# Kernel optimization log

Measured on AMD Instinct MI355X. Metric: run time of the kernel, lower is better.

The kernel has to match this reference:

```python
import jax, jax.numpy as jnp
import numpy as np

N = 8192          # tokens
CD = 512          # coarse_dim
FD = 512          # fine_dim
CB = 4096         # coarse codebook size
FB = 8192         # fine codebook size
COST = 0.25       # commitment cost
LRELU = 0.1
EPS = 1e-5


def _vq(x, emb):
    # squared-distance cdist: [n, K]
    d = jnp.sum(x * x, axis=1, keepdims=True) + jnp.sum(emb * emb, axis=1) - 2.0 * (x @ emb.T)
    idx = jnp.argmin(d, axis=1)          # temperature=1.0 (updates=0); scaling doesn't change argmin
    q = emb[idx]                          # gather == one-hot @ emb, without materializing one-hot
    e_loss = jnp.mean((jax.lax.stop_gradient(q) - x) ** 2)
    q_loss = jnp.mean((q - jax.lax.stop_gradient(x)) ** 2)
    loss = q_loss + COST * e_loss
    q_st = x + jax.lax.stop_gradient(q - x)   # straight-through
    return q_st, loss


def _mlp(x, w, b, g, be):
    # Linear (torch: x @ W.T + b) -> LayerNorm -> LeakyReLU(0.1)
    h = x @ w.T + b
    m = jnp.mean(h, axis=-1, keepdims=True)
    v = jnp.var(h, axis=-1, keepdims=True)
    h = (h - m) / jnp.sqrt(v + EPS) * g + be
    return jnp.where(h > 0, h, LRELU * h)


def setup_inputs() -> dict:
    key = jax.random.key(0)
    ks = jax.random.split(key, 6)
    xav_c = float(np.sqrt(6.0 / (CB + CD)))
    xav_f = float(np.sqrt(6.0 / (FB + FD)))
    lin_s = float(np.sqrt(1.0 / CD))
    return {
        'z': jax.random.normal(ks[0], (N, CD + FD), dtype=jnp.float32),
        'coarse_emb': jax.random.uniform(ks[1], (CB, CD), jnp.float32, -xav_c, xav_c),
        'fine_emb': jax.random.uniform(ks[2], (FB, FD), jnp.float32, -xav_f, xav_f),
        'w_c2f': jax.random.uniform(ks[3], (FD, CD), jnp.float32, -lin_s, lin_s),
        'b_c2f': jnp.zeros((FD,), jnp.float32),
        'g_c2f': jnp.ones((FD,), jnp.float32),
        'be_c2f': jnp.zeros((FD,), jnp.float32),
        'w_f2c': jax.random.uniform(ks[4], (CD, FD), jnp.float32, -lin_s, lin_s),
        'b_f2c': jnp.zeros((CD,), jnp.float32),
        'g_f2c': jnp.ones((CD,), jnp.float32),
        'be_f2c': jnp.zeros((CD,), jnp.float32),
        'gate_c_raw': jnp.float32(0.5),
        'gate_f_raw': jnp.float32(0.5),
    }


def reference(z, coarse_emb, fine_emb, w_c2f, b_c2f, g_c2f, be_c2f,
              w_f2c, b_f2c, g_f2c, be_f2c, gate_c_raw, gate_f_raw):
    split = z.shape[1] // 2
    z_coarse, z_fine = z[:, :split], z[:, split:]

    z_coarse_q, coarse_loss = _vq(z_coarse, coarse_emb)
    coarse_influence = _mlp(jax.lax.stop_gradient(z_coarse_q), w_c2f, b_c2f, g_c2f, be_c2f)
    gate_c = jax.nn.sigmoid(gate_c_raw)

    residual = z_fine - gate_c * coarse_influence
    z_fine_q, fine_loss = _vq(residual, fine_emb)

    fine_feedback = _mlp(jax.lax.stop_gradient(z_fine_q), w_f2c, b_f2c, g_f2c, be_f2c)
    gate_f = jax.nn.sigmoid(gate_f_raw)

    z_coarse_corrected = z_coarse_q + 0.1 * gate_f * fine_feedback
    z_fine_reconstructed = z_fine_q + gate_c * coarse_influence
    z_hierarchical = jnp.concatenate([z_coarse_corrected, z_fine_reconstructed], axis=1)
    vq_loss = coarse_loss + fine_loss
    return z_hierarchical, vq_loss
```

## Files before the change

kernel.cpp:

```cpp
#include <hip/hip_runtime.h>
#include <hip/hip_bf16.h>
#include <cstdint>
#include <cstddef>

#define KD 512

#define OFF_CN   0u
#define OFF_FN   16384u
#define OFF_ZN   49152u
#define OFF_RN   81920u
#define OFF_LOSS 114688u
#define OFF_AMC  114944u
#define OFF_AMF  180480u
#define OFF_CEH  246016u
#define OFF_CEL  4440320u
#define OFF_FEH  8634624u
#define OFF_FEL  17023232u
#define OFF_ZCH  25411840u
#define OFF_ZCL  33800448u
#define OFF_RH   42189056u
#define OFF_RL   50577664u
#define OFF_W1H  58966272u
#define OFF_W1L  59490560u
#define OFF_W2H  60014848u
#define OFF_W2L  60539136u
#define OFF_H    61063424u
#define OFF_INFL 77840640u


typedef __attribute__((ext_vector_type(8))) short bf16x8;
typedef __attribute__((ext_vector_type(4))) float f32x4;
typedef unsigned long long u64;

__device__ __forceinline__ bf16x8 as_bf16x8(int4 v) {
  union { int4 i; bf16x8 b; } u; u.i = v; return u.b;
}

__device__ __forceinline__ void gl_lds16(const void* g, void* l) {
  __builtin_amdgcn_global_load_lds(
      (const __attribute__((address_space(1))) void*)g,
      (__attribute__((address_space(3))) void*)l, 16, 0, 0);
}

__device__ __forceinline__ float block_sum(float v, float* sred) {
#pragma unroll
  for (int off = 32; off > 0; off >>= 1) v += __shfl_down(v, off, 64);
  if ((threadIdx.x & 63) == 0) sred[threadIdx.x >> 6] = v;
  __syncthreads();
  float r = sred[0] + sred[1] + sred[2] + sred[3];
  __syncthreads();
  return r;
}

__device__ __forceinline__ float sigmoidf_(float x) { return 1.0f / (1.0f + expf(-x)); }

__device__ __forceinline__ void split_bf16(float v, __hip_bfloat16* hi, __hip_bfloat16* lo) {
  __hip_bfloat16 h = __float2bfloat16(v);
  *hi = h;
  *lo = __float2bfloat16(v - __bfloat162float(h));
}

__device__ __forceinline__ unsigned enc_sortable(float f) {
  unsigned u = __float_as_uint(f);
  return (u & 0x80000000u) ? ~u : (u | 0x80000000u);
}
__device__ __forceinline__ float dec_sortable(unsigned ub) {
  unsigned o = (ub & 0x80000000u) ? (ub & 0x7fffffffu) : ~ub;
  return __uint_as_float(o);
}
__device__ __forceinline__ u64 umin64(u64 a, u64 b) { return a < b ? a : b; }
__device__ __forceinline__ u64 umax64(u64 a, u64 b) { return a > b ? a : b; }

__device__ __forceinline__ void merge3(u64& a1, u64& a2, u64& a3, u64 b1, u64 b2, u64 b3) {
  u64 p = umax64(a1, b1);
  u64 q = umin64(a2, b2);
  u64 r = umax64(a2, b2);
  u64 s = umin64(a3, b3);
  u64 m1 = umin64(a1, b1);
  u64 m2 = umin64(p, q);
  u64 m3 = umin64(umin64(umax64(p, q), r), s);
  a1 = m1; a2 = m2; a3 = m3;
}

__global__ __launch_bounds__(256) void prep(
    const float* __restrict__ ce, const float* __restrict__ fe, const float* __restrict__ z,
    const float* __restrict__ w1, const float* __restrict__ w2,
    float* __restrict__ cn, float* __restrict__ fn, float* __restrict__ zn,
    __hip_bfloat16* __restrict__ ceH, __hip_bfloat16* __restrict__ ceL,
    __hip_bfloat16* __restrict__ feH, __hip_bfloat16* __restrict__ feL,
    __hip_bfloat16* __restrict__ zcH,
    __hip_bfloat16* __restrict__ w1H, __hip_bfloat16* __restrict__ w1L,
    __hip_bfloat16* __restrict__ w2H, __hip_bfloat16* __restrict__ w2L,
    float* __restrict__ lossp) {
  __shared__ float sred[4];
  const int b = blockIdx.x, t = threadIdx.x;
  const float* src;
  float* nd = nullptr;
  __hip_bfloat16 *dh = nullptr, *dl = nullptr;
  int fragMode = 0, hiOnly = 0;
  size_t row;
  if (b < 4096) {
    row = b; src = ce + row * KD; nd = cn + row; dh = ceH; dl = ceL; fragMode = 1;
  } else if (b < 12288) {
    row = b - 4096; src = fe + row * KD; nd = fn + row; dh = feH; dl = feL; fragMode = 1;
  } else if (b < 20480) {
    row = b - 12288; src = z + row * 1024; nd = zn + row; dh = zcH; hiOnly = 1;
  } else if (b < 20992) {
    row = b - 20480; src = w1 + row * KD; dh = w1H; dl = w1L;
  } else {
    row = b - 20992; src = w2 + row * KD; dh = w2H; dl = w2L;
  }
  float acc = 0.0f;
  if (fragMode) {
    float v0 = src[t], v1 = src[t + 256];
    acc = v0 * v0 + v1 * v1;
  } else {
#pragma unroll
    for (int j = 0; j < 2; ++j) {
      int c = t + j * 256;
      float v = src[c];
      acc += v * v;
      __hip_bfloat16 h, l;
      split_bf16(v, &h, &l);
      dh[row * KD + c] = h;
      if (!hiOnly) dl[row * KD + c] = l;
    }
  }
  if (nd) {
    float s = block_sum(acc, sred);
    if (t == 0) nd[0] = s;
  } else {
    __syncthreads();
    __syncthreads();
  }
  if (fragMode && t < 64) {
    union { int4 i; __hip_bfloat16 s[8]; } ph, pl;
#pragma unroll
    for (int j = 0; j < 8; ++j) {
      float v = src[8 * t + j];
      split_bf16(v, &ph.s[j], &pl.s[j]);
    }
    const int chunkIdx = (int)(((row >> 4) * 16 + (t >> 2)) * 64 +
                               ((size_t)((t & 3) << 4) | (row & 15)));
    ((int4*)dh)[chunkIdx] = ph.i;
    ((int4*)dl)[chunkIdx] = pl.i;
  }
  if (b == 20480 && t == 0) lossp[0] = 0.0f;
}

__global__ __launch_bounds__(256, 2) void vq10(
    const int4* __restrict__ AfH,
    const __hip_bfloat16* __restrict__ Bh,
    const float* __restrict__ cn,
    u64* __restrict__ bkeys) {
  __shared__ __align__(16) int4 sA[3][1024];
  __shared__ __align__(16) __hip_bfloat16 sB[3][128 * 32];
  const int t = threadIdx.x;
  const int w = t >> 6, l = t & 63;

  const int bx = blockIdx.x;
  const int by = blockIdx.y;
  const int rowTile = by << 8;
  const int colTile = bx << 7;
  const int NB = gridDim.y;

  const int rl = l >> 2;
  const int sbp = (l & 3) ^ ((l >> 3) & 3);
  const size_t gOff0 = (size_t)(colTile + (w << 5) + rl) * KD + (sbp << 3);
  const size_t gOff1 = gOff0 + (size_t)16 * KD;
  const int lOffB0 = (w << 5) << 5;
  const int lOffB1 = lOffB0 + (16 << 5);

  const int rtg = rowTile >> 4;
  const int aS0 = ((rtg + 4 * w + 0) << 10) + l;
  const int aS1 = ((rtg + 4 * w + 1) << 10) + l;
  const int aS2 = ((rtg + 4 * w + 2) << 10) + l;
  const int aS3 = ((rtg + 4 * w + 3) << 10) + l;

  const int fr = l & 15;
  const int q = l >> 4;

  f32x4 acc[4][8];
#pragma unroll
  for (int i = 0; i < 4; ++i)
#pragma unroll
    for (int j = 0; j < 8; ++j) acc[i][j] = (f32x4){0.f, 0.f, 0.f, 0.f};

#define STAGE(ck) do {                                                   \
    const int sl_ = (ck) % 3;                                            \
    gl_lds16(AfH + aS0 + ((ck) << 6), &sA[sl_][(4 * w + 0) << 6]);       \
    gl_lds16(AfH + aS1 + ((ck) << 6), &sA[sl_][(4 * w + 1) << 6]);       \
    gl_lds16(AfH + aS2 + ((ck) << 6), &sA[sl_][(4 * w + 2) << 6]);       \
    gl_lds16(AfH + aS3 + ((ck) << 6), &sA[sl_][(4 * w + 3) << 6]);       \
    gl_lds16(Bh + gOff0 + ((size_t)(ck) << 5), &sB[sl_][lOffB0]);        \
    gl_lds16(Bh + gOff1 + ((size_t)(ck) << 5), &sB[sl_][lOffB1]);        \
  } while (0)

  STAGE(0);
  STAGE(1);
  __builtin_amdgcn_sched_barrier(0);

#pragma unroll
  for (int i = 0; i < 16; ++i) {
    if (i < 15) asm volatile("s_waitcnt vmcnt(6) lgkmcnt(0)" ::: "memory");
    else        asm volatile("s_waitcnt vmcnt(0) lgkmcnt(0)" ::: "memory");
    __builtin_amdgcn_s_barrier();
    __builtin_amdgcn_sched_barrier(0);
    if (i + 2 < 16) STAGE(i + 2);
    __builtin_amdgcn_sched_barrier(0);

    const int cb = i % 3;
    bf16x8 afh[4], bfh[8];
#pragma unroll
    for (int mt = 0; mt < 4; ++mt)
      afh[mt] = as_bf16x8(sA[cb][((4 * w) + mt) * 64 + l]);
#pragma unroll
    for (int nt = 0; nt < 8; ++nt) {
      const int rB = (nt << 4) + fr;
      const int o = (rB << 5) + ((q ^ ((rB >> 1) & 3)) << 3);
      bfh[nt] = *(const bf16x8*)(sB[cb] + o);
    }
    __builtin_amdgcn_s_setprio(1);
#pragma unroll
    for (int mt = 0; mt < 4; ++mt)
#pragma unroll
      for (int nt = 0; nt < 8; ++nt)
        acc[mt][nt] = __builtin_amdgcn_mfma_f32_16x16x32_bf16(afh[mt], bfh[nt], acc[mt][nt], 0, 0, 0);
    __builtin_amdgcn_s_setprio(0);
  }
#undef STAGE

  u64 tk1[8], tk2[8], tk3[8];
#pragma unroll
  for (int nt = 0; nt < 8; ++nt) {
    u64 t1 = ~0ULL, t2 = ~0ULL, t3 = ~0ULL;
#pragma unroll
    for (int mt = 0; mt < 4; ++mt) {
#pragma unroll
      for (int reg = 0; reg < 4; ++reg) {
        const int code = rowTile + (w << 6) + (mt << 4) + (q << 2) + reg;
        float d = cn[code] - 2.0f * acc[mt][nt][reg];
        u64 key = ((u64)enc_sortable(d) << 32) | (u64)(unsigned)code;
        if (key < t1) { t3 = t2; t2 = t1; t1 = key; }
        else if (key < t2) { t3 = t2; t2 = key; }
        else if (key < t3) { t3 = key; }
      }
    }
#pragma unroll
    for (int off = 16; off <= 32; off <<= 1) {
      u64 b1 = __shfl_xor(t1, off, 64);
      u64 b2 = __shfl_xor(t2, off, 64);
      u64 b3 = __shfl_xor(t3, off, 64);
      merge3(t1, t2, t3, b1, b2, b3);
    }
    tk1[nt] = t1; tk2[nt] = t2; tk3[nt] = t3;
  }

  __syncthreads();
  u64* sk = (u64*)sA;
  if (w > 0 && l < 16) {
#pragma unroll
    for (int nt = 0; nt < 8; ++nt) {
      const int o = (((w << 3) + nt) * 16 + fr) * 3;
      sk[o] = tk1[nt]; sk[o + 1] = tk2[nt]; sk[o + 2] = tk3[nt];
    }
  }
  __syncthreads();
  if (w == 0 && l < 16) {
#pragma unroll
    for (int nt = 0; nt < 8; ++nt) {
      u64 t1 = tk1[nt], t2 = tk2[nt], t3 = tk3[nt];
#pragma unroll
      for (int wv = 1; wv < 4; ++wv) {
        const int o = (((wv << 3) + nt) * 16 + fr) * 3;
        merge3(t1, t2, t3, sk[o], sk[o + 1], sk[o + 2]);
      }
      const int query = colTile + (nt << 4) + fr;
      const size_t bo = ((size_t)query * NB + by) * 3;
      bkeys[bo] = t1; bkeys[bo + 1] = t2; bkeys[bo + 2] = t3;
    }
  }
}

__global__ __launch_bounds__(256) void rescue(
    const u64* __restrict__ bkeys, int NB3,
    const float* __restrict__ Q, int qStride,
    const float* __restrict__ Cb,
    const float* __restrict__ qn, const float* __restrict__ cnorm,
    float dscale, u64* __restrict__ am) {
  const int wv = threadIdx.x >> 6, l = threadIdx.x & 63;
  const int qi = (blockIdx.x << 2) + wv;
  const u64* kq = bkeys + (size_t)qi * NB3;
  u64 kk[3];
#pragma unroll
  for (int j = 0; j < 3; ++j) {
    const int idx = l + (j << 6);
    kk[j] = (idx < NB3) ? kq[idx] : ~0ULL;
  }
  u64 kmin = umin64(kk[0], umin64(kk[1], kk[2]));
#pragma unroll
  for (int off = 32; off > 0; off >>= 1) kmin = umin64(kmin, __shfl_xor(kmin, off, 64));
  const float xnv = qn[qi];
  const float dmin = dec_sortable((unsigned)(kmin >> 32));
  const float thr = dmin + dscale * sqrtf(xnv) + 0.01f;
  const u64 thrKey = ((u64)enc_sortable(thr) << 32) | 0xffffffffULL;

  const float* qrow = Q + (size_t)qi * qStride;
  const float4 qa = *(const float4*)(qrow + (l << 3));
  const float4 qb = *(const float4*)(qrow + (l << 3) + 4);
  float bestD = 3.4e38f;
  int bestC = 0x7fffffff;
#pragma unroll
  for (int j = 0; j < 3; ++j) {
    bool pend = kk[j] <= thrKey;
    u64 mask;
    while ((mask = __ballot(pend)) != 0ULL) {
      const int src = __ffsll((unsigned long long)mask) - 1;
      const u64 key = __shfl(kk[j], src, 64);
      if (l == src) pend = false;
      const int code = (int)(unsigned)(key & 0xffffffffULL);
      const float* crow = Cb + (size_t)code * KD;
      const float4 ca = *(const float4*)(crow + (l << 3));
      const float4 cb = *(const float4*)(crow + (l << 3) + 4);
      float dt = qa.x * ca.x + qa.y * ca.y + qa.z * ca.z + qa.w * ca.w +
                 qb.x * cb.x + qb.y * cb.y + qb.z * cb.z + qb.w * cb.w;
#pragma unroll
      for (int off = 32; off > 0; off >>= 1) dt += __shfl_xor(dt, off, 64);
      const float d = (xnv + cnorm[code]) - 2.0f * dt;
      if (d < bestD || (d == bestD && code < bestC)) { bestD = d; bestC = code; }
    }
  }
  if (l == 0) am[qi] = ((u64)enc_sortable(bestD) << 32) | (unsigned)bestC;
}

__global__ __launch_bounds__(256) void mlp6(
    const int4* __restrict__ AfH, const int4* __restrict__ AfL,
    const u64* __restrict__ gather,
    const __hip_bfloat16* __restrict__ Bh, const __hip_bfloat16* __restrict__ Bl,
    const float* __restrict__ bias, float* __restrict__ C) {
  __shared__ __align__(16) __hip_bfloat16 sAh[128 * 32];
  __shared__ __align__(16) __hip_bfloat16 sAl[128 * 32];
  __shared__ __align__(16) __hip_bfloat16 sBh[128 * 32];
  __shared__ __align__(16) __hip_bfloat16 sBl[128 * 32];
  const int t = threadIdx.x;
  const int w = t >> 6, l = t & 63;
  const int rowTile = blockIdx.y << 7;
  const int colTile = blockIdx.x << 7;
  const int wr = (w >> 1) << 6;
  const int wc = (w & 1) << 6;

  const int srow = t >> 2;
  const int sb = t & 3;
  const int skE = sb << 3;
  const int swz = (sb ^ ((srow >> 1) & 3)) << 3;
  const int wOff0 = (srow << 5) + swz;
  const int wOff1 = ((srow + 64) << 5) + swz;

  unsigned i0 = ((const unsigned*)gather)[2 * (rowTile + srow)];
  unsigned i1 = ((const unsigned*)gather)[2 * (rowTile + 64 + srow)];
  const int a0 = (int)((i0 >> 4) << 10) + (sb << 4) + (int)(i0 & 15);
  const int a1 = (int)((i1 >> 4) << 10) + (sb << 4) + (int)(i1 & 15);
  const size_t br0 = (size_t)(colTile + srow) * KD;
  const size_t br1 = (size_t)(colTile + 64 + srow) * KD;

  const int fr = l & 15;
  const int q = l >> 4;

  f32x4 acc[4][4];
#pragma unroll
  for (int i = 0; i < 4; ++i)
#pragma unroll
    for (int j = 0; j < 4; ++j) acc[i][j] = (f32x4){0.f, 0.f, 0.f, 0.f};

  for (int kk = 0; kk < KD; kk += 32) {
    const int kc64 = (kk >> 5) << 6;
    int4 vAh0 = AfH[a0 + kc64];
    int4 vAh1 = AfH[a1 + kc64];
    int4 vAl0 = AfL[a0 + kc64];
    int4 vAl1 = AfL[a1 + kc64];
    int4 vBh0 = *(const int4*)(Bh + br0 + kk + skE);
    int4 vBh1 = *(const int4*)(Bh + br1 + kk + skE);
    int4 vBl0 = *(const int4*)(Bl + br0 + kk + skE);
    int4 vBl1 = *(const int4*)(Bl + br1 + kk + skE);
    __syncthreads();
    *(int4*)(sAh + wOff0) = vAh0; *(int4*)(sAh + wOff1) = vAh1;
    *(int4*)(sAl + wOff0) = vAl0; *(int4*)(sAl + wOff1) = vAl1;
    *(int4*)(sBh + wOff0) = vBh0; *(int4*)(sBh + wOff1) = vBh1;
    *(int4*)(sBl + wOff0) = vBl0; *(int4*)(sBl + wOff1) = vBl1;
    __syncthreads();

    bf16x8 afh[4], afl[4], bfh[4], bfl[4];
#pragma unroll
    for (int mt = 0; mt < 4; ++mt) {
      const int rA = wr + (mt << 4) + fr;
      const int o = (rA << 5) + ((q ^ ((rA >> 1) & 3)) << 3);
      afh[mt] = *(const bf16x8*)(sAh + o);
      afl[mt] = *(const bf16x8*)(sAl + o);
    }
#pragma unroll
    for (int nt = 0; nt < 4; ++nt) {
      const int rB = wc + (nt << 4) + fr;
      const int o = (rB << 5) + ((q ^ ((rB >> 1) & 3)) << 3);
      bfh[nt] = *(const bf16x8*)(sBh + o);
      bfl[nt] = *(const bf16x8*)(sBl + o);
    }
#pragma unroll
    for (int mt = 0; mt < 4; ++mt)
#pragma unroll
      for (int nt = 0; nt < 4; ++nt) {
        acc[mt][nt] = __builtin_amdgcn_mfma_f32_16x16x32_bf16(afh[mt], bfh[nt], acc[mt][nt], 0, 0, 0);
        acc[mt][nt] = __builtin_amdgcn_mfma_f32_16x16x32_bf16(afh[mt], bfl[nt], acc[mt][nt], 0, 0, 0);
        acc[mt][nt] = __builtin_amdgcn_mfma_f32_16x16x32_bf16(afl[mt], bfh[nt], acc[mt][nt], 0, 0, 0);
      }
  }

  const int quad = l >> 4;
#pragma unroll
  for (int mt = 0; mt < 4; ++mt) {
#pragma unroll
    for (int reg = 0; reg < 4; ++reg) {
      const int row = rowTile + wr + (mt << 4) + (quad << 2) + reg;
#pragma unroll
      for (int nt = 0; nt < 4; ++nt) {
        const int col = colTile + wc + (nt << 4) + fr;
        C[(size_t)row * KD + col] = acc[mt][nt][reg] + bias[col];
      }
    }
  }
}

__global__ __launch_bounds__(256) void ln_residual(
    const float* __restrict__ h, const float* __restrict__ g, const float* __restrict__ be,
    const float* __restrict__ z, const float* __restrict__ gRaw,
    __hip_bfloat16* __restrict__ infl, float* __restrict__ rn,
    __hip_bfloat16* __restrict__ rH, float* __restrict__ resF) {
  __shared__ float sred[4];
  const int row = blockIdx.x, t = threadIdx.x;
  const size_t base = (size_t)row * KD;
  float h0 = h[base + t], h1 = h[base + t + 256];
  float m = block_sum(h0 + h1, sred) * (1.0f / 512.0f);
  float d0 = h0 - m, d1 = h1 - m;
  float var = block_sum(d0 * d0 + d1 * d1, sred) * (1.0f / 512.0f);
  float sq = sqrtf(var + 1e-5f);
  float gc = sigmoidf_(gRaw[0]);
  float v0 = d0 / sq * g[t] + be[t];
  float v1 = d1 / sq * g[t + 256] + be[t + 256];
  v0 = v0 > 0.0f ? v0 : 0.1f * v0;
  v1 = v1 > 0.0f ? v1 : 0.1f * v1;
  infl[base + t] = __float2bfloat16(v0);
  infl[base + t + 256] = __float2bfloat16(v1);
  float zf0 = z[(size_t)row * 1024 + 512 + t];
  float zf1 = z[(size_t)row * 1024 + 512 + t + 256];
  float r0 = zf0 - gc * v0, r1 = zf1 - gc * v1;
  rH[base + t] = __float2bfloat16(r0);
  rH[base + t + 256] = __float2bfloat16(r1);
  resF[base + t] = r0;
  resF[base + t + 256] = r1;
  float rs = block_sum(r0 * r0 + r1 * r1, sred);
  if (t == 0) rn[row] = rs;
}

__global__ __launch_bounds__(256) void finalize(
    const float* __restrict__ h, const float* __restrict__ g, const float* __restrict__ be,
    const __hip_bfloat16* __restrict__ infl,
    const u64* __restrict__ amc, const u64* __restrict__ amf,
    const float* __restrict__ z, const float* __restrict__ ce, const float* __restrict__ fe,
    const float* __restrict__ gcRaw, const float* __restrict__ gfRaw,
    float* __restrict__ out, float* __restrict__ lossp) {
  __shared__ float sred[4];
  const int row = blockIdx.x, t = threadIdx.x;
  const size_t base = (size_t)row * KD;
  float h0 = h[base + t], h1 = h[base + t + 256];
  float m = block_sum(h0 + h1, sred) * (1.0f / 512.0f);
  float d0 = h0 - m, d1 = h1 - m;
  float var = block_sum(d0 * d0 + d1 * d1, sred) * (1.0f / 512.0f);
  float sq = sqrtf(var + 1e-5f);
  float fb0 = d0 / sq * g[t] + be[t];
  float fb1 = d1 / sq * g[t + 256] + be[t + 256];
  fb0 = fb0 > 0.0f ? fb0 : 0.1f * fb0;
  fb1 = fb1 > 0.0f ? fb1 : 0.1f * fb1;
  float gc = sigmoidf_(gcRaw[0]);
  float gf = sigmoidf_(gfRaw[0]);
  unsigned ic = (unsigned)(amc[row] & 0xffffffffULL);
  unsigned ifx = (unsigned)(amf[row] & 0xffffffffULL);
  float loc = 0.0f;
#pragma unroll
  for (int j = 0; j < 2; ++j) {
    int c = t + j * 256;
    float fb = j ? fb1 : fb0;
    float qc = ce[(size_t)ic * KD + c];
    float qf = fe[(size_t)ifx * KD + c];
    float zc = z[(size_t)row * 1024 + c];
    float zf = z[(size_t)row * 1024 + 512 + c];
    float fl = __bfloat162float(infl[base + c]);
    out[(size_t)row * 1024 + c] = qc + 0.1f * gf * fb;
    out[(size_t)row * 1024 + 512 + c] = qf + gc * fl;
    float dc = qc - zc;
    float res = zf - gc * fl;
    float df = qf - res;
    loc += dc * dc + df * df;
  }
  float ls = block_sum(loc, sred);
  if (t == 0) atomicAdd(lossp, ls);
}

__global__ void loss_write(const float* __restrict__ lossp, float* __restrict__ out) {
  out[0] = 1.25f * lossp[0] / (8192.0f * 512.0f);
}

extern "C" void kernel_launch(void* const* d_in, const int* in_sizes, int n_in,
                              void* d_out, int out_size, void* d_ws, size_t ws_size,
                              hipStream_t stream) {
  const float* z      = (const float*)d_in[0];
  const float* ce     = (const float*)d_in[1];
  const float* fe     = (const float*)d_in[2];
  const float* w_c2f  = (const float*)d_in[3];
  const float* b_c2f  = (const float*)d_in[4];
  const float* g_c2f  = (const float*)d_in[5];
  const float* be_c2f = (const float*)d_in[6];
  const float* w_f2c  = (const float*)d_in[7];
  const float* b_f2c  = (const float*)d_in[8];
  const float* g_f2c  = (const float*)d_in[9];
  const float* be_f2c = (const float*)d_in[10];
  const float* gcRaw  = (const float*)d_in[11];
  const float* gfRaw  = (const float*)d_in[12];
  float* out = (float*)d_out;
  char* ws = (char*)d_ws;

  float* cn = (float*)(ws + OFF_CN);
  float* fn = (float*)(ws + OFF_FN);
  float* zn = (float*)(ws + OFF_ZN);
  float* rn = (float*)(ws + OFF_RN);
  float* lossp = (float*)(ws + OFF_LOSS);
  u64* amc = (u64*)(ws + OFF_AMC);
  u64* amf = (u64*)(ws + OFF_AMF);
  __hip_bfloat16* ceH = (__hip_bfloat16*)(ws + OFF_CEH);
  __hip_bfloat16* ceL = (__hip_bfloat16*)(ws + OFF_CEL);
  __hip_bfloat16* feH = (__hip_bfloat16*)(ws + OFF_FEH);
  __hip_bfloat16* feL = (__hip_bfloat16*)(ws + OFF_FEL);
  __hip_bfloat16* zcH = (__hip_bfloat16*)(ws + OFF_ZCH);
  __hip_bfloat16* rH  = (__hip_bfloat16*)(ws + OFF_RH);
  __hip_bfloat16* w1H = (__hip_bfloat16*)(ws + OFF_W1H);
  __hip_bfloat16* w1L = (__hip_bfloat16*)(ws + OFF_W1L);
  __hip_bfloat16* w2H = (__hip_bfloat16*)(ws + OFF_W2H);
  __hip_bfloat16* w2L = (__hip_bfloat16*)(ws + OFF_W2L);
  float* h = (float*)(ws + OFF_H);
  __hip_bfloat16* infl = (__hip_bfloat16*)(ws + OFF_INFL);
  u64* bkeys = (u64*)(ws + OFF_H);
  float* resF = (float*)(ws + OFF_ZCH);

  prep<<<21504, 256, 0, stream>>>(ce, fe, z, w_c2f, w_f2c, cn, fn, zn,
                                  ceH, ceL, feH, feL, zcH,
                                  w1H, w1L, w2H, w2L, lossp);

  vq10<<<dim3(64, 16), 256, 0, stream>>>((const int4*)ceH, zcH, cn, bkeys);

  rescue<<<2048, 256, 0, stream>>>(bkeys, 48, z, 1024, ce, zn, cn, 0.00321f, amc);

  mlp6<<<dim3(4, 64), 256, 0, stream>>>((const int4*)ceH, (const int4*)ceL, amc,
                                        w1H, w1L, b_c2f, h);

  ln_residual<<<8192, 256, 0, stream>>>(h, g_c2f, be_c2f, z, gcRaw, infl, rn, rH, resF);

  vq10<<<dim3(64, 32), 256, 0, stream>>>((const int4*)feH, rH, fn, bkeys);

  rescue<<<2048, 256, 0, stream>>>(bkeys, 96, resF, 512, fe, rn, fn, 0.00233f, amf);

  mlp6<<<dim3(4, 64), 256, 0, stream>>>((const int4*)feH, (const int4*)feL, amf,
                                        w2H, w2L, b_f2c, h);

  finalize<<<8192, 256, 0, stream>>>(h, g_f2c, be_f2c, infl, amc, amf, z, ce, fe,
                                     gcRaw, gfRaw, out, lossp);
  loss_write<<<1, 1, 0, stream>>>(lossp, out + (size_t)8192 * 1024);
}
```

Before: 545.8 us.

## Load VQ distance operands as pre-swizzled MFMA fragments straight from global memory

Both operands of the VQ distance GEMM (token activations and residuals) are now stored in the MFMA fragment layout. vq11 reads them directly from global memory into registers with register double buffering, with no LDS staging, async LDS loads or block barriers. The fine-stage feedback MLP becomes a single-pass bf16 GEMM (mlp1p) that drops the low-order correction terms. The risks are higher register pressure, global-load latency that LDS no longer hides, and lower precision in the fine feedback MLP.

```diff
diff --git a/kernel.cpp b/kernel.cpp
--- a/kernel.cpp
+++ b/kernel.cpp
@@ -36,12 +36,6 @@
   union { int4 i; bf16x8 b; } u; u.i = v; return u.b;
 }
 
-__device__ __forceinline__ void gl_lds16(const void* g, void* l) {
-  __builtin_amdgcn_global_load_lds(
-      (const __attribute__((address_space(1))) void*)g,
-      (__attribute__((address_space(3))) void*)l, 16, 0, 0);
-}
-
 __device__ __forceinline__ float block_sum(float v, float* sred) {
 #pragma unroll
   for (int off = 32; off > 0; off >>= 1) v += __shfl_down(v, off, 64);
@@ -88,7 +82,7 @@
     float* __restrict__ cn, float* __restrict__ fn, float* __restrict__ zn,
     __hip_bfloat16* __restrict__ ceH, __hip_bfloat16* __restrict__ ceL,
     __hip_bfloat16* __restrict__ feH, __hip_bfloat16* __restrict__ feL,
-    __hip_bfloat16* __restrict__ zcH,
+    __hip_bfloat16* __restrict__ zcF,
     __hip_bfloat16* __restrict__ w1H, __hip_bfloat16* __restrict__ w1L,
     __hip_bfloat16* __restrict__ w2H, __hip_bfloat16* __restrict__ w2L,
     float* __restrict__ lossp) {
@@ -104,7 +98,7 @@
   } else if (b < 12288) {
     row = b - 4096; src = fe + row * KD; nd = fn + row; dh = feH; dl = feL; fragMode = 1;
   } else if (b < 20480) {
-    row = b - 12288; src = z + row * 1024; nd = zn + row; dh = zcH; hiOnly = 1;
+    row = b - 12288; src = z + row * 1024; nd = zn + row; dh = zcF; fragMode = 1; hiOnly = 1;
   } else if (b < 20992) {
     row = b - 20480; src = w1 + row * KD; dh = w1H; dl = w1L;
   } else {
@@ -113,7 +107,12 @@
   float acc = 0.0f;
   if (fragMode) {
     float v0 = src[t], v1 = src[t + 256];
-    acc = v0 * v0 + v1 * v1;
+    if (hiOnly) {
+      acc = v0 * v0;
+      acc += v1 * v1;
+    } else {
+      acc = v0 * v0 + v1 * v1;
+    }
   } else {
 #pragma unroll
     for (int j = 0; j < 2; ++j) {
@@ -123,7 +122,7 @@
       __hip_bfloat16 h, l;
       split_bf16(v, &h, &l);
       dh[row * KD + c] = h;
-      if (!hiOnly) dl[row * KD + c] = l;
+      dl[row * KD + c] = l;
     }
   }
   if (nd) {
@@ -143,39 +142,31 @@
     const int chunkIdx = (int)(((row >> 4) * 16 + (t >> 2)) * 64 +
                                ((size_t)((t & 3) << 4) | (row & 15)));
     ((int4*)dh)[chunkIdx] = ph.i;
-    ((int4*)dl)[chunkIdx] = pl.i;
+    if (!hiOnly) ((int4*)dl)[chunkIdx] = pl.i;
   }
   if (b == 20480 && t == 0) lossp[0] = 0.0f;
 }
 
-__global__ __launch_bounds__(256, 2) void vq10(
+__global__ __launch_bounds__(256, 2) void vq11(
     const int4* __restrict__ AfH,
-    const __hip_bfloat16* __restrict__ Bh,
+    const int4* __restrict__ BfH,
     const float* __restrict__ cn,
     u64* __restrict__ bkeys) {
-  __shared__ __align__(16) int4 sA[3][1024];
-  __shared__ __align__(16) __hip_bfloat16 sB[3][128 * 32];
+  __shared__ u64 sk[1536];
   const int t = threadIdx.x;
   const int w = t >> 6, l = t & 63;
-
-  const int bx = blockIdx.x;
-  const int by = blockIdx.y;
+  const int bx = blockIdx.x, by = blockIdx.y;
   const int rowTile = by << 8;
   const int colTile = bx << 7;
   const int NB = gridDim.y;
 
-  const int rl = l >> 2;
-  const int sbp = (l & 3) ^ ((l >> 3) & 3);
-  const size_t gOff0 = (size_t)(colTile + (w << 5) + rl) * KD + (sbp << 3);
-  const size_t gOff1 = gOff0 + (size_t)16 * KD;
-  const int lOffB0 = (w << 5) << 5;
-  const int lOffB1 = lOffB0 + (16 << 5);
-
   const int rtg = rowTile >> 4;
-  const int aS0 = ((rtg + 4 * w + 0) << 10) + l;
-  const int aS1 = ((rtg + 4 * w + 1) << 10) + l;
-  const int aS2 = ((rtg + 4 * w + 2) << 10) + l;
-  const int aS3 = ((rtg + 4 * w + 3) << 10) + l;
+  const int ctg = colTile >> 4;
+  int aB[4], bB[8];
+#pragma unroll
+  for (int mt = 0; mt < 4; ++mt) aB[mt] = ((rtg + (w << 2) + mt) << 10) + l;
+#pragma unroll
+  for (int nt = 0; nt < 8; ++nt) bB[nt] = ((ctg + nt) << 10) + l;
 
   const int fr = l & 15;
   const int q = l >> 4;
@@ -186,49 +177,37 @@
 #pragma unroll
     for (int j = 0; j < 8; ++j) acc[i][j] = (f32x4){0.f, 0.f, 0.f, 0.f};
 
-#define STAGE(ck) do {                                                   \
-    const int sl_ = (ck) % 3;                                            \
-    gl_lds16(AfH + aS0 + ((ck) << 6), &sA[sl_][(4 * w + 0) << 6]);       \
-    gl_lds16(AfH + aS1 + ((ck) << 6), &sA[sl_][(4 * w + 1) << 6]);       \
-    gl_lds16(AfH + aS2 + ((ck) << 6), &sA[sl_][(4 * w + 2) << 6]);       \
-    gl_lds16(AfH + aS3 + ((ck) << 6), &sA[sl_][(4 * w + 3) << 6]);       \
-    gl_lds16(Bh + gOff0 + ((size_t)(ck) << 5), &sB[sl_][lOffB0]);        \
-    gl_lds16(Bh + gOff1 + ((size_t)(ck) << 5), &sB[sl_][lOffB1]);        \
-  } while (0)
-
-  STAGE(0);
-  STAGE(1);
-  __builtin_amdgcn_sched_barrier(0);
+  int4 a0[4], b0[8];
+#pragma unroll
+  for (int mt = 0; mt < 4; ++mt) a0[mt] = AfH[aB[mt]];
+#pragma unroll
+  for (int nt = 0; nt < 8; ++nt) b0[nt] = BfH[bB[nt]];
 
 #pragma unroll
   for (int i = 0; i < 16; ++i) {
-    if (i < 15) asm volatile("s_waitcnt vmcnt(6) lgkmcnt(0)" ::: "memory");
-    else        asm volatile("s_waitcnt vmcnt(0) lgkmcnt(0)" ::: "memory");
-    __builtin_amdgcn_s_barrier();
-    __builtin_amdgcn_sched_barrier(0);
-    if (i + 2 < 16) STAGE(i + 2);
-    __builtin_amdgcn_sched_barrier(0);
-
-    const int cb = i % 3;
-    bf16x8 afh[4], bfh[8];
-#pragma unroll
-    for (int mt = 0; mt < 4; ++mt)
-      afh[mt] = as_bf16x8(sA[cb][((4 * w) + mt) * 64 + l]);
-#pragma unroll
-    for (int nt = 0; nt < 8; ++nt) {
-      const int rB = (nt << 4) + fr;
-      const int o = (rB << 5) + ((q ^ ((rB >> 1) & 3)) << 3);
-      bfh[nt] = *(const bf16x8*)(sB[cb] + o);
+    int4 a1[4], b1[8];
+    if (i + 1 < 16) {
+#pragma unroll
+      for (int mt = 0; mt < 4; ++mt) a1[mt] = AfH[aB[mt] + ((i + 1) << 6)];
+#pragma unroll
+      for (int nt = 0; nt < 8; ++nt) b1[nt] = BfH[bB[nt] + ((i + 1) << 6)];
     }
     __builtin_amdgcn_s_setprio(1);
 #pragma unroll
-    for (int mt = 0; mt < 4; ++mt)
+    for (int mt = 0; mt < 4; ++mt) {
+      const bf16x8 af = as_bf16x8(a0[mt]);
 #pragma unroll
       for (int nt = 0; nt < 8; ++nt)
-        acc[mt][nt] = __builtin_amdgcn_mfma_f32_16x16x32_bf16(afh[mt], bfh[nt], acc[mt][nt], 0, 0, 0);
+        acc[mt][nt] = __builtin_amdgcn_mfma_f32_16x16x32_bf16(af, as_bf16x8(b0[nt]), acc[mt][nt], 0, 0, 0);
+    }
     __builtin_amdgcn_s_setprio(0);
-  }
-#undef STAGE
+    if (i + 1 < 16) {
+#pragma unroll
+      for (int mt = 0; mt < 4; ++mt) a0[mt] = a1[mt];
+#pragma unroll
+      for (int nt = 0; nt < 8; ++nt) b0[nt] = b1[nt];
+    }
+  }
 
   u64 tk1[8], tk2[8], tk3[8];
 #pragma unroll
@@ -257,7 +236,6 @@
   }
 
   __syncthreads();
-  u64* sk = (u64*)sA;
   if (w > 0 && l < 16) {
 #pragma unroll
     for (int nt = 0; nt < 8; ++nt) {
@@ -429,12 +407,96 @@
   }
 }
 
+__global__ __launch_bounds__(256) void mlp1p(
+    const int4* __restrict__ AfH,
+    const u64* __restrict__ gather,
+    const __hip_bfloat16* __restrict__ Bh,
+    const float* __restrict__ bias, float* __restrict__ C) {
+  __shared__ __align__(16) __hip_bfloat16 sAh[128 * 32];
+  __shared__ __align__(16) __hip_bfloat16 sBh[128 * 32];
+  const int t = threadIdx.x;
+  const int w = t >> 6, l = t & 63;
+  const int rowTile = blockIdx.y << 7;
+  const int colTile = blockIdx.x << 7;
+  const int wr = (w >> 1) << 6;
+  const int wc = (w & 1) << 6;
+
+  const int srow = t >> 2;
+  const int sb = t & 3;
+  const int skE = sb << 3;
+  const int swz = (sb ^ ((srow >> 1) & 3)) << 3;
+  const int wOff0 = (srow << 5) + swz;
+  const int wOff1 = ((srow + 64) << 5) + swz;
+
+  unsigned i0 = ((const unsigned*)gather)[2 * (rowTile + srow)];
+  unsigned i1 = ((const unsigned*)gather)[2 * (rowTile + 64 + srow)];
+  const int a0 = (int)((i0 >> 4) << 10) + (sb << 4) + (int)(i0 & 15);
+  const int a1 = (int)((i1 >> 4) << 10) + (sb << 4) + (int)(i1 & 15);
+  const size_t br0 = (size_t)(colTile + srow) * KD;
+  const size_t br1 = (size_t)(colTile + 64 + srow) * KD;
+
+  const int fr = l & 15;
+  const int q = l >> 4;
+
+  f32x4 acc[4][4];
+#pragma unroll
+  for (int i = 0; i < 4; ++i)
+#pragma unroll
+    for (int j = 0; j < 4; ++j) acc[i][j] = (f32x4){0.f, 0.f, 0.f, 0.f};
+
+  for (int kk = 0; kk < KD; kk += 32) {
+    const int kc64 = (kk >> 5) << 6;
+    int4 vAh0 = AfH[a0 + kc64];
+    int4 vAh1 = AfH[a1 + kc64];
+    int4 vBh0 = *(const int4*)(Bh + br0 + kk + skE);
+    int4 vBh1 = *(const int4*)(Bh + br1 + kk + skE);
+    __syncthreads();
+    *(int4*)(sAh + wOff0) = vAh0; *(int4*)(sAh + wOff1) = vAh1;
+    *(int4*)(sBh + wOff0) = vBh0; *(int4*)(sBh + wOff1) = vBh1;
+    __syncthreads();
+
+    bf16x8 afh[4], bfh[4];
+#pragma unroll
+    for (int mt = 0; mt < 4; ++mt) {
+      const int rA = wr + (mt << 4) + fr;
+      const int o = (rA << 5) + ((q ^ ((rA >> 1) & 3)) << 3);
+      afh[mt] = *(const bf16x8*)(sAh + o);
+    }
+#pragma unroll
+    for (int nt = 0; nt < 4; ++nt) {
+      const int rB = wc + (nt << 4) + fr;
+      const int o = (rB << 5) + ((q ^ ((rB >> 1) & 3)) << 3);
+      bfh[nt] = *(const bf16x8*)(sBh + o);
+    }
+#pragma unroll
+    for (int mt = 0; mt < 4; ++mt)
+#pragma unroll
+      for (int nt = 0; nt < 4; ++nt)
+        acc[mt][nt] = __builtin_amdgcn_mfma_f32_16x16x32_bf16(afh[mt], bfh[nt], acc[mt][nt], 0, 0, 0);
+  }
+
+  const int quad = l >> 4;
+#pragma unroll
+  for (int mt = 0; mt < 4; ++mt) {
+#pragma unroll
+    for (int reg = 0; reg < 4; ++reg) {
+      const int row = rowTile + wr + (mt << 4) + (quad << 2) + reg;
+#pragma unroll
+      for (int nt = 0; nt < 4; ++nt) {
+        const int col = colTile + wc + (nt << 4) + fr;
+        C[(size_t)row * KD + col] = acc[mt][nt][reg] + bias[col];
+      }
+    }
+  }
+}
+
 __global__ __launch_bounds__(256) void ln_residual(
     const float* __restrict__ h, const float* __restrict__ g, const float* __restrict__ be,
     const float* __restrict__ z, const float* __restrict__ gRaw,
     __hip_bfloat16* __restrict__ infl, float* __restrict__ rn,
-    __hip_bfloat16* __restrict__ rH, float* __restrict__ resF) {
+    __hip_bfloat16* __restrict__ rF, float* __restrict__ resF) {
   __shared__ float sred[4];
+  __shared__ float sr[512];
   const int row = blockIdx.x, t = threadIdx.x;
   const size_t base = (size_t)row * KD;
   float h0 = h[base + t], h1 = h[base + t + 256];
@@ -452,12 +514,19 @@
   float zf0 = z[(size_t)row * 1024 + 512 + t];
   float zf1 = z[(size_t)row * 1024 + 512 + t + 256];
   float r0 = zf0 - gc * v0, r1 = zf1 - gc * v1;
-  rH[base + t] = __float2bfloat16(r0);
-  rH[base + t + 256] = __float2bfloat16(r1);
+  sr[t] = r0; sr[t + 256] = r1;
   resF[base + t] = r0;
   resF[base + t + 256] = r1;
   float rs = block_sum(r0 * r0 + r1 * r1, sred);
   if (t == 0) rn[row] = rs;
+  if (t < 64) {
+    union { int4 i; __hip_bfloat16 s[8]; } ph;
+#pragma unroll
+    for (int j = 0; j < 8; ++j) ph.s[j] = __float2bfloat16(sr[8 * t + j]);
+    const int chunkIdx = (int)(((row >> 4) * 16 + (t >> 2)) * 64 +
+                               ((size_t)((t & 3) << 4) | (row & 15)));
+    ((int4*)rF)[chunkIdx] = ph.i;
+  }
 }
 
 __global__ __launch_bounds__(256) void finalize(
@@ -538,8 +607,8 @@
   __hip_bfloat16* ceL = (__hip_bfloat16*)(ws + OFF_CEL);
   __hip_bfloat16* feH = (__hip_bfloat16*)(ws + OFF_FEH);
   __hip_bfloat16* feL = (__hip_bfloat16*)(ws + OFF_FEL);
-  __hip_bfloat16* zcH = (__hip_bfloat16*)(ws + OFF_ZCH);
-  __hip_bfloat16* rH  = (__hip_bfloat16*)(ws + OFF_RH);
+  __hip_bfloat16* zcF = (__hip_bfloat16*)(ws + OFF_ZCH);
+  __hip_bfloat16* rF  = (__hip_bfloat16*)(ws + OFF_RH);
   __hip_bfloat16* w1H = (__hip_bfloat16*)(ws + OFF_W1H);
   __hip_bfloat16* w1L = (__hip_bfloat16*)(ws + OFF_W1L);
   __hip_bfloat16* w2H = (__hip_bfloat16*)(ws + OFF_W2H);
@@ -550,24 +619,23 @@
   float* resF = (float*)(ws + OFF_ZCH);
 
   prep<<<21504, 256, 0, stream>>>(ce, fe, z, w_c2f, w_f2c, cn, fn, zn,
-                                  ceH, ceL, feH, feL, zcH,
+                                  ceH, ceL, feH, feL, zcF,
                                   w1H, w1L, w2H, w2L, lossp);
 
-  vq10<<<dim3(64, 16), 256, 0, stream>>>((const int4*)ceH, zcH, cn, bkeys);
+  vq11<<<dim3(64, 16), 256, 0, stream>>>((const int4*)ceH, (const int4*)zcF, cn, bkeys);
 
   rescue<<<2048, 256, 0, stream>>>(bkeys, 48, z, 1024, ce, zn, cn, 0.00321f, amc);
 
   mlp6<<<dim3(4, 64), 256, 0, stream>>>((const int4*)ceH, (const int4*)ceL, amc,
                                         w1H, w1L, b_c2f, h);
 
-  ln_residual<<<8192, 256, 0, stream>>>(h, g_c2f, be_c2f, z, gcRaw, infl, rn, rH, resF);
-
-  vq10<<<dim3(64, 32), 256, 0, stream>>>((const int4*)feH, rH, fn, bkeys);
+  ln_residual<<<8192, 256, 0, stream>>>(h, g_c2f, be_c2f, z, gcRaw, infl, rn, rF, resF);
+
+  vq11<<<dim3(64, 32), 256, 0, stream>>>((const int4*)feH, (const int4*)rF, fn, bkeys);
 
   rescue<<<2048, 256, 0, stream>>>(bkeys, 96, resF, 512, fe, rn, fn, 0.00233f, amf);
 
-  mlp6<<<dim3(4, 64), 256, 0, stream>>>((const int4*)feH, (const int4*)feL, amf,
-                                        w2H, w2L, b_f2c, h);
+  mlp1p<<<dim3(4, 64), 256, 0, stream>>>((const int4*)feH, amf, w2H, b_f2c, h);
 
   finalize<<<8192, 256, 0, stream>>>(h, g_f2c, be_f2c, infl, amc, amf, z, ce, fe,
                                      gcRaw, gfRaw, out, lossp);
```

After: 627.4 us. 1.15x slower.
